# Kernel optimization log

Measured on AMD Instinct MI355X. Metric: run time of the kernel, lower is better.

Reference implementation:

```python
import jax, jax.numpy as jnp
import numpy as np

B, I, H = 16384, 512, 512
HH = H // 2


def _lrelu(v):
    return jnp.where(v > 0, v, 0.01 * v)


def setup_inputs() -> dict:
    key = jax.random.key(0)
    ks = jax.random.split(key, 20)
    s = 1.0 / np.sqrt(H)
    rn = lambda k, shp, sc: (jax.random.normal(k, shp, jnp.float32) * sc)
    return {
        "x": rn(ks[0], (B, I), 1.0),
        "h0": rn(ks[1], (1, B, H), 1.0),
        "c0": rn(ks[2], (1, B, H), 1.0),
        "cum": jax.random.uniform(ks[3], (B, 1), jnp.float32),
        # LSTM params (torch gate order i, f, g, o)
        "W_ih": rn(ks[4], (4 * H, I), s),
        "W_hh": rn(ks[5], (4 * H, H), s),
        "b_ih": rn(ks[6], (4 * H,), s),
        "b_hh": rn(ks[7], (4 * H,), s),
        # skip gate MLP
        "W_sp": rn(ks[8], (HH, H), s),
        "b_sp": rn(ks[9], (HH,), s),
        "W_sc": rn(ks[10], (HH, H), s),
        "b_sc": rn(ks[11], (HH,), s),
        "W_so": rn(ks[12], (1, HH), s),
        "b_so": rn(ks[13], (1,), s),
        # threshold gate MLP
        "W_tp": rn(ks[14], (HH, H), s),
        "b_tp": rn(ks[15], (HH,), s),
        "W_to": rn(ks[16], (1, HH), s),
        "b_to": rn(ks[17], (1,), s),
    }


def reference(x, h0, c0, cum, W_ih, W_hh, b_ih, b_hh,
              W_sp, b_sp, W_sc, b_sc, W_so, b_so,
              W_tp, b_tp, W_to, b_to):
    # single-step, single-layer LSTM
    gates = x @ W_ih.T + b_ih + h0[0] @ W_hh.T + b_hh  # [B, 4H]
    i_g, f_g, g_g, o_g = jnp.split(gates, 4, axis=-1)
    i_g = jax.nn.sigmoid(i_g)
    f_g = jax.nn.sigmoid(f_g)
    g_g = jnp.tanh(g_g)
    o_g = jax.nn.sigmoid(o_g)
    c1l = f_g * c0[0] + i_g * g_g          # [B, H]
    h1l = o_g * jnp.tanh(c1l)              # [B, H]
    h1, c1 = h1l[None], c1l[None]          # [1, B, H]

    # skip gate: delta prob from c0[-1], c1[-1]
    sg = _lrelu(c0[-1] @ W_sp.T + b_sp + c1[-1] @ W_sc.T + b_sc)  # [B, H/2]
    update_prob_delta = jax.nn.sigmoid(sg @ W_so.T + b_so)        # [B, 1]

    # threshold gate from c0[-1]
    tg = _lrelu(c0[-1] @ W_tp.T + b_tp)                           # [B, H/2]
    update_threshold = jax.nn.sigmoid(tg @ W_to.T + b_to)         # [B, 1]

    update_prob = cum + jnp.minimum(update_prob_delta, 1.0 - cum)  # [B, 1]
    # straight-through round: fwd hard threshold, bwd identity to prob
    hard = (update_prob > update_threshold).astype(jnp.float32)
    update_gate = update_prob + jax.lax.stop_gradient(hard - update_prob)

    new_h = update_gate * h1 + (1.0 - update_gate) * h0  # [1, B, H]
    new_c = update_gate * c1 + (1.0 - update_gate) * c0  # [1, B, H]
    update_cum = (1.0 - update_gate) * update_prob        # [B, 1]
    return (new_h, new_c, update_cum, update_prob_delta, update_prob)
```

## Files before the change

### kernel.cpp

```cpp
#include <hip/hip_runtime.h>
#include <math.h>

#define BB 16384
#define HH 512

typedef short short8 __attribute__((ext_vector_type(8)));
typedef float f32x4 __attribute__((ext_vector_type(4)));
typedef unsigned short ushort_t;

__device__ __forceinline__ float sigm(float v){ return 1.0f/(1.0f+expf(-v)); }

__device__ __forceinline__ unsigned short f2bf(float f){
    unsigned int u = __float_as_uint(f);
    u = u + 0x7FFFu + ((u>>16)&1u);
    return (unsigned short)(u>>16);
}
__device__ __forceinline__ float bf2f(unsigned short h){
    return __uint_as_float(((unsigned int)h)<<16);
}
__device__ __forceinline__ void gll16(const void* g, void* l){
    __builtin_amdgcn_global_load_lds((const __attribute__((address_space(1))) void*)g,
                                     (__attribute__((address_space(3))) void*)l, 16, 0, 0);
}

__global__ void k_prep_A(const float* __restrict__ x, const float* __restrict__ h0,
                         ushort_t* __restrict__ A1h, ushort_t* __restrict__ A1l)
{
    int u = blockIdx.x*256 + threadIdx.x;
    int r  = u & 255;
    int c  = (u >> 8) & 3;
    int kt = (u >> 10) & 31;
    int tm = u >> 15;
    int row = tm*256 + r;
    int k0 = kt*32 + c*8;
    const float* src = (k0 < 512) ? (x + (size_t)row*512 + k0)
                                  : (h0 + (size_t)row*512 + (k0-512));
    float4 v0 = *(const float4*)(src);
    float4 v1 = *(const float4*)(src+4);
    float vv[8] = {v0.x,v0.y,v0.z,v0.w,v1.x,v1.y,v1.z,v1.w};
    short8 hi, lo;
#pragma unroll
    for (int j=0;j<8;++j){
        unsigned short h = f2bf(vv[j]);
        unsigned short l = f2bf(vv[j] - bf2f(h));
        hi[j] = (short)h; lo[j] = (short)l;
    }
    size_t off = (size_t)u * 8;
    *(short8*)(A1h + off) = hi;
    *(short8*)(A1l + off) = lo;
}

__global__ void k_prep_A2(const float* __restrict__ c0,
                          ushort_t* __restrict__ A2h, ushort_t* __restrict__ A2l)
{
    int u = blockIdx.x*256 + threadIdx.x;
    int r  = u & 127;
    int c  = (u >> 7) & 3;
    int tk = (u >> 9) & 15;
    int tm = u >> 13;
    int row = tm*128 + r;
    int k0 = tk*32 + c*8;
    const float* src = c0 + (size_t)row*512 + k0;
    float4 v0 = *(const float4*)(src);
    float4 v1 = *(const float4*)(src+4);
    float vv[8] = {v0.x,v0.y,v0.z,v0.w,v1.x,v1.y,v1.z,v1.w};
    short8 hi, lo;
#pragma unroll
    for (int j=0;j<8;++j){
        unsigned short h = f2bf(vv[j]);
        unsigned short l = f2bf(vv[j] - bf2f(h));
        hi[j] = (short)h; lo[j] = (short)l;
    }
    size_t off = ((size_t)tm*32 + tk)*4096 + (size_t)(c*128 + r)*8;
    *(short8*)(A2h + off) = hi;
    *(short8*)(A2l + off) = lo;
}

__global__ void k_prep_B(const float* __restrict__ W_ih, const float* __restrict__ W_hh,
                         const float* __restrict__ b_ih, const float* __restrict__ b_hh,
                         ushort_t* __restrict__ B1h, ushort_t* __restrict__ B1l,
                         float* __restrict__ bgp)
{
    int u = blockIdx.x*256 + threadIdx.x;
    int r  = u & 255;
    int c  = (u >> 8) & 3;
    int kt = (u >> 10) & 31;
    int tn = u >> 15;
    int g = (r>>4)&3;
    int h = tn*64 + (r>>6)*16 + (r&15);
    int wrow = g*512 + h;
    int k0 = kt*32 + c*8;
    const float* src = (k0 < 512) ? (W_ih + (size_t)wrow*512 + k0)
                                  : (W_hh + (size_t)wrow*512 + (k0-512));
    float4 v0 = *(const float4*)(src);
    float4 v1 = *(const float4*)(src+4);
    float vv[8] = {v0.x,v0.y,v0.z,v0.w,v1.x,v1.y,v1.z,v1.w};
    short8 hi, lo;
#pragma unroll
    for (int j=0;j<8;++j){
        unsigned short hq = f2bf(vv[j]);
        unsigned short lq = f2bf(vv[j] - bf2f(hq));
        hi[j] = (short)hq; lo[j] = (short)lq;
    }
    size_t off = (size_t)u * 8;
    *(short8*)(B1h + off) = hi;
    *(short8*)(B1l + off) = lo;
    if (kt == 0 && c == 0) bgp[tn*256 + r] = b_ih[wrow] + b_hh[wrow];
}

__global__ void k_prep_B2(const float* __restrict__ W_sp, const float* __restrict__ W_sc,
                          const float* __restrict__ W_tp,
                          const float* __restrict__ b_sp, const float* __restrict__ b_sc,
                          const float* __restrict__ b_tp,
                          ushort_t* __restrict__ B2h, ushort_t* __restrict__ B2l,
                          float* __restrict__ bs2)
{
    int u = blockIdx.x*256 + threadIdx.x;
    int r  = u & 127;
    int c  = (u >> 7) & 3;
    int tk = (u >> 9) & 31;
    int tn = u >> 14;
    int n = tn*128 + r;
    int k0 = tk*32 + c*8;
    float vv[8];
    if (n < 256) {
        const float* src = (k0 < 512) ? (W_sp + (size_t)n*512 + k0)
                                      : (W_sc + (size_t)n*512 + (k0-512));
        float4 v0 = *(const float4*)(src);
        float4 v1 = *(const float4*)(src+4);
        vv[0]=v0.x; vv[1]=v0.y; vv[2]=v0.z; vv[3]=v0.w;
        vv[4]=v1.x; vv[5]=v1.y; vv[6]=v1.z; vv[7]=v1.w;
    } else if (k0 < 512) {
        const float* src = W_tp + (size_t)(n-256)*512 + k0;
        float4 v0 = *(const float4*)(src);
        float4 v1 = *(const float4*)(src+4);
        vv[0]=v0.x; vv[1]=v0.y; vv[2]=v0.z; vv[3]=v0.w;
        vv[4]=v1.x; vv[5]=v1.y; vv[6]=v1.z; vv[7]=v1.w;
    } else {
#pragma unroll
        for (int j=0;j<8;++j) vv[j] = 0.0f;
    }
    short8 hi, lo;
#pragma unroll
    for (int j=0;j<8;++j){
        unsigned short hq = f2bf(vv[j]);
        unsigned short lq = f2bf(vv[j] - bf2f(hq));
        hi[j] = (short)hq; lo[j] = (short)lq;
    }
    size_t off = (size_t)u * 8;
    *(short8*)(B2h + off) = hi;
    *(short8*)(B2l + off) = lo;
    if (tk == 0 && c == 0) bs2[n] = (n < 256) ? (b_sp[n] + b_sc[n]) : b_tp[n-256];
}

#define STEP(T, DO_STAGE, VMASM)                                                     \
  {                                                                                  \
    ushort_t* bufA = &lds[(T) & 3][0];                                               \
    ushort_t* bufB = &lds[(T) & 3][8192];                                            \
    short8 bf[4], af[4];                                                             \
    _Pragma("unroll") for (int fn = 0; fn < 4; ++fn)                                 \
        bf[fn] = *(const short8*)&bufB[boff[fn]];                                    \
    _Pragma("unroll") for (int fm = 0; fm < 4; ++fm)                                 \
        af[fm] = *(const short8*)&bufA[aoff[fm]];                                    \
    if (DO_STAGE) {                                                                  \
        const int uu = (T) + 3;                                                      \
        const ushort_t* As_ = ((uu >> 5) == 1) ? Al : Ah;                            \
        size_t ga = ((size_t)tm*32 + (uu & 31))*8192 + (size_t)tid*8;                \
        ushort_t* dA = &lds[uu & 3][0];                                              \
        gll16(As_ + ga,        dA + tid*8);                                          \
        gll16(As_ + ga + 4096, dA + 4096 + tid*8);                                   \
    }                                                                                \
    asm volatile("s_barrier" ::: "memory");                                          \
    asm volatile("s_waitcnt lgkmcnt(0)" ::: "memory");                               \
    __builtin_amdgcn_sched_barrier(0);                                               \
    __builtin_amdgcn_s_setprio(1);                                                   \
    _Pragma("unroll") for (int fm = 0; fm < 4; ++fm)                                 \
        _Pragma("unroll") for (int fn = 0; fn < 4; ++fn)                             \
            acc[fm][fn] = __builtin_amdgcn_mfma_f32_16x16x32_bf16(af[fm], bf[fn], acc[fm][fn], 0,0,0); \
    __builtin_amdgcn_s_setprio(0);                                                   \
    asm volatile("s_barrier" ::: "memory");                                          \
    short8 af2[4];                                                                   \
    _Pragma("unroll") for (int fm = 0; fm < 4; ++fm)                                 \
        af2[fm] = *(const short8*)&bufA[aoff[4+fm]];                                 \
    if (DO_STAGE) {                                                                  \
        const int uu = (T) + 3;                                                      \
        const ushort_t* Bs_ = ((uu >> 5) == 2) ? Bl : Bh;                            \
        size_t gb = ((size_t)tn*32 + (uu & 31))*8192 + (size_t)tid*8;                \
        ushort_t* dB = &lds[uu & 3][8192];                                           \
        gll16(Bs_ + gb,        dB + tid*8);                                          \
        gll16(Bs_ + gb + 4096, dB + 4096 + tid*8);                                   \
    }                                                                                \
    VMASM;                                                                           \
    asm volatile("s_barrier" ::: "memory");                                          \
    asm volatile("s_waitcnt lgkmcnt(0)" ::: "memory");                               \
    __builtin_amdgcn_sched_barrier(0);                                               \
    __builtin_amdgcn_s_setprio(1);                                                   \
    _Pragma("unroll") for (int fm = 0; fm < 4; ++fm)                                 \
        _Pragma("unroll") for (int fn = 0; fn < 4; ++fn)                             \
            acc[4+fm][fn] = __builtin_amdgcn_mfma_f32_16x16x32_bf16(af2[fm], bf[fn], acc[4+fm][fn], 0,0,0); \
    __builtin_amdgcn_s_setprio(0);                                                   \
    asm volatile("s_barrier" ::: "memory");                                          \
  }

__global__ __launch_bounds__(512, 2) void k_gemm_gates(
    const ushort_t* __restrict__ Ah, const ushort_t* __restrict__ Al,
    const ushort_t* __restrict__ Bh, const ushort_t* __restrict__ Bl,
    const float* __restrict__ bgp, const float* __restrict__ c0,
    float* __restrict__ outH, float* __restrict__ outC,
    ushort_t* __restrict__ A2h, ushort_t* __restrict__ A2l)
{
    __shared__ __align__(16) ushort_t lds[4][16384];
    const int tid  = threadIdx.x;
    const int lane = tid & 63;
    const int wid  = tid >> 6;
    const int wr   = wid >> 2;
    const int wc   = wid & 3;
    const int l15  = lane & 15;
    const int lq   = lane >> 4;
    const int bid  = (int)blockIdx.x;
    const int v    = (bid & 7)*64 + (bid >> 3);
    const int tm   = v >> 3;
    const int tn   = v & 7;

    f32x4 acc[8][4];
#pragma unroll
    for (int fn = 0; fn < 4; ++fn) {
        float bv = bgp[tn*256 + wc*64 + fn*16 + l15];
#pragma unroll
        for (int fm = 0; fm < 8; ++fm) {
            acc[fm][fn][0]=bv; acc[fm][fn][1]=bv; acc[fm][fn][2]=bv; acc[fm][fn][3]=bv;
        }
    }

    int aoff[8], boff[4];
#pragma unroll
    for (int f = 0; f < 8; ++f) aoff[f] = (lq*256 + wr*128 + f*16 + l15) * 8;
#pragma unroll
    for (int f = 0; f < 4; ++f) boff[f] = (lq*256 + wc*64 + f*16 + l15) * 8;

#pragma unroll
    for (int u0 = 0; u0 < 3; ++u0) {
        size_t ga = ((size_t)tm*32 + u0)*8192 + (size_t)tid*8;
        size_t gb = ((size_t)tn*32 + u0)*8192 + (size_t)tid*8;
        gll16(Ah + ga,        &lds[u0][0]     + tid*8);
        gll16(Ah + ga + 4096, &lds[u0][4096]  + tid*8);
        gll16(Bh + gb,        &lds[u0][8192]  + tid*8);
        gll16(Bh + gb + 4096, &lds[u0][12288] + tid*8);
    }
    asm volatile("s_waitcnt vmcnt(8)" ::: "memory");
    asm volatile("s_barrier" ::: "memory");

    for (int t = 0; t < 93; ++t) {
        STEP(t, 1, asm volatile("s_waitcnt vmcnt(8)" ::: "memory"));
    }
    STEP(93, 0, asm volatile("s_waitcnt vmcnt(4)" ::: "memory"));
    STEP(94, 0, asm volatile("s_waitcnt vmcnt(0)" ::: "memory"));
    STEP(95, 0, ((void)0));

    const int h = tn*64 + wc*16 + l15;
#pragma unroll
    for (int fm = 0; fm < 8; ++fm) {
        int row0 = tm*256 + wr*128 + fm*16 + lq*4;
#pragma unroll
        for (int r = 0; r < 4; ++r) {
            int row = row0 + r;
            size_t idx = (size_t)row*512 + h;
            float ig = sigm(acc[fm][0][r]);
            float fg = sigm(acc[fm][1][r]);
            float gg = tanhf(acc[fm][2][r]);
            float og = sigm(acc[fm][3][r]);
            float c1 = fg*c0[idx] + ig*gg;
            float h1 = og*tanhf(c1);
            outC[idx] = c1;
            outH[idx] = h1;
            unsigned short ch = f2bf(c1);
            unsigned short cl = f2bf(c1 - bf2f(ch));
            size_t a2 = ((size_t)(row>>7)*32 + 16 + (h>>5))*4096
                      + (size_t)((((h>>3)&3))*128 + (row&127))*8 + (h&7);
            A2h[a2] = ch;
            A2l[a2] = cl;
        }
    }
}

__global__ __launch_bounds__(256) void k_gemm_sgtg(
    const ushort_t* __restrict__ Ah, const ushort_t* __restrict__ Al,
    const ushort_t* __restrict__ Bh, const ushort_t* __restrict__ Bl,
    const float* __restrict__ bs2,
    float* __restrict__ sgtg)
{
    __shared__ __align__(16) ushort_t AsH[4096];
    __shared__ __align__(16) ushort_t AsL[4096];
    __shared__ __align__(16) ushort_t BsH[4096];
    __shared__ __align__(16) ushort_t BsL[4096];
    const int tid = threadIdx.x;
    const int lane = tid & 63;
    const int wid = tid >> 6;
    const int wr = wid >> 1, wc = wid & 1;
    const int bid = (int)blockIdx.x;
    const int v = (bid & 7)*64 + (bid >> 3);
    const int tm = v >> 2;
    const int tn = v & 3;
    const int l15 = lane & 15;
    const int lq = lane >> 4;

    f32x4 acc[4][4];
#pragma unroll
    for (int fn = 0; fn < 4; ++fn) {
        float bv = bs2[tn*128 + wc*64 + fn*16 + l15];
#pragma unroll
        for (int fm = 0; fm < 4; ++fm) {
            acc[fm][fn][0]=bv; acc[fm][fn][1]=bv; acc[fm][fn][2]=bv; acc[fm][fn][3]=bv;
        }
    }

    const size_t baseA = (size_t)tm * (32*4096);
    const size_t baseB = (size_t)tn * (32*4096);
    int aoff[4], boff[4];
#pragma unroll
    for (int f = 0; f < 4; ++f) {
        aoff[f] = (lq*128 + wr*64 + f*16 + l15) * 8;
        boff[f] = (lq*128 + wc*64 + f*16 + l15) * 8;
    }
    const int si = wid * 2;

    for (int tk = 0; tk < 32; ++tk) {
        size_t ga = baseA + (size_t)tk*4096 + (size_t)lane*8;
        size_t gb = baseB + (size_t)tk*4096 + (size_t)lane*8;
#pragma unroll
        for (int t = 0; t < 2; ++t) {
            int i = si + t;
            gll16(Ah + ga + i*512, AsH + i*512);
            gll16(Al + ga + i*512, AsL + i*512);
            gll16(Bh + gb + i*512, BsH + i*512);
            gll16(Bl + gb + i*512, BsL + i*512);
        }
        __syncthreads();
        short8 bhv[4], blv[4];
#pragma unroll
        for (int fn = 0; fn < 4; ++fn) {
            bhv[fn] = *(const short8*)&BsH[boff[fn]];
            blv[fn] = *(const short8*)&BsL[boff[fn]];
        }
#pragma unroll
        for (int fm = 0; fm < 4; ++fm) {
            short8 ahv = *(const short8*)&AsH[aoff[fm]];
            short8 alv = *(const short8*)&AsL[aoff[fm]];
#pragma unroll
            for (int fn = 0; fn < 4; ++fn) {
                acc[fm][fn] = __builtin_amdgcn_mfma_f32_16x16x32_bf16(ahv, bhv[fn], acc[fm][fn], 0,0,0);
                acc[fm][fn] = __builtin_amdgcn_mfma_f32_16x16x32_bf16(alv, bhv[fn], acc[fm][fn], 0,0,0);
                acc[fm][fn] = __builtin_amdgcn_mfma_f32_16x16x32_bf16(ahv, blv[fn], acc[fm][fn], 0,0,0);
            }
        }
        __syncthreads();
    }

#pragma unroll
    for (int fm = 0; fm < 4; ++fm) {
        int row0 = tm*128 + wr*64 + fm*16 + lq*4;
#pragma unroll
        for (int fn = 0; fn < 4; ++fn) {
            int n = tn*128 + wc*64 + fn*16 + l15;
#pragma unroll
            for (int r = 0; r < 4; ++r) {
                int row = row0 + r;
                float vv = acc[fm][fn][r];
                vv = vv > 0.f ? vv : 0.01f*vv;
                sgtg[(size_t)row*512 + n] = vv;
            }
        }
    }
}

__global__ __launch_bounds__(256) void k_final(
    const float* __restrict__ sgtg,
    const float* __restrict__ h0, const float* __restrict__ c0,
    const float* __restrict__ cum,
    const float* __restrict__ W_so, const float* __restrict__ b_so,
    const float* __restrict__ W_to, const float* __restrict__ b_to,
    float* __restrict__ outH, float* __restrict__ outC,
    float* __restrict__ outCum, float* __restrict__ outDelta, float* __restrict__ outProb)
{
    int w = threadIdx.x >> 6;
    int lane = threadIdx.x & 63;
    int b = blockIdx.x * 4 + w;
    const float* row = sgtg + (size_t)b * 512;
    float so = 0.f, to = 0.f;
#pragma unroll
    for (int u = 0; u < 4; ++u) {
        int c = lane + 64 * u;
        so = fmaf(row[c], W_so[c], so);
        to = fmaf(row[256 + c], W_to[c], to);
    }
#pragma unroll
    for (int off = 32; off; off >>= 1) {
        so += __shfl_down(so, off);
        to += __shfl_down(to, off);
    }
    so = __shfl(so, 0);
    to = __shfl(to, 0);
    float delta = sigm(so + b_so[0]);
    float thr   = sigm(to + b_to[0]);
    float cu = cum[b];
    float prob = cu + fminf(delta, 1.0f - cu);
    float hard = (prob > thr) ? 1.0f : 0.0f;
    if (lane == 0) {
        outDelta[b] = delta;
        outProb[b]  = prob;
        outCum[b]   = (1.0f - hard) * prob;
    }
    if (hard == 0.0f) {
#pragma unroll
        for (int u = 0; u < 8; ++u) {
            size_t idx = (size_t)b * 512 + lane + 64 * u;
            outH[idx] = h0[idx];
            outC[idx] = c0[idx];
        }
    }
}

extern "C" void kernel_launch(void* const* d_in, const int* in_sizes, int n_in,
                              void* d_out, int out_size, void* d_ws, size_t ws_size,
                              hipStream_t stream)
{
    const float* x    = (const float*)d_in[0];
    const float* h0   = (const float*)d_in[1];
    const float* c0   = (const float*)d_in[2];
    const float* cum  = (const float*)d_in[3];
    const float* W_ih = (const float*)d_in[4];
    const float* W_hh = (const float*)d_in[5];
    const float* b_ih = (const float*)d_in[6];
    const float* b_hh = (const float*)d_in[7];
    const float* W_sp = (const float*)d_in[8];
    const float* b_sp = (const float*)d_in[9];
    const float* W_sc = (const float*)d_in[10];
    const float* b_sc = (const float*)d_in[11];
    const float* W_so = (const float*)d_in[12];
    const float* b_so = (const float*)d_in[13];
    const float* W_tp = (const float*)d_in[14];
    const float* b_tp = (const float*)d_in[15];
    const float* W_to = (const float*)d_in[16];
    const float* b_to = (const float*)d_in[17];

    float* out      = (float*)d_out;
    float* outH     = out;
    float* outC     = out + (size_t)BB * HH;
    float* outCum   = out + (size_t)2 * BB * HH;
    float* outDelta = outCum + BB;
    float* outProb  = outDelta + BB;

    char* w = (char*)d_ws;
    ushort_t* A1h = (ushort_t*)(w);
    ushort_t* A1l = (ushort_t*)(w + 33554432ull);
    ushort_t* A2h = (ushort_t*)(w + 67108864ull);
    ushort_t* A2l = (ushort_t*)(w + 100663296ull);
    ushort_t* B1h = (ushort_t*)(w + 134217728ull);
    ushort_t* B1l = (ushort_t*)(w + 138412032ull);
    ushort_t* B2h = (ushort_t*)(w + 142606336ull);
    ushort_t* B2l = (ushort_t*)(w + 143654912ull);
    float*    bgp = (float*)(w + 144703488ull);
    float*    bs2 = (float*)(w + 144711680ull);
    float*    sgtg = (float*)A1h;

    k_prep_A <<<8192, 256, 0, stream>>>(x, h0, A1h, A1l);
    k_prep_A2<<<4096, 256, 0, stream>>>(c0, A2h, A2l);
    k_prep_B <<<1024, 256, 0, stream>>>(W_ih, W_hh, b_ih, b_hh, B1h, B1l, bgp);
    k_prep_B2<<<256, 256, 0, stream>>>(W_sp, W_sc, W_tp, b_sp, b_sc, b_tp, B2h, B2l, bs2);
    k_gemm_gates<<<512, 512, 0, stream>>>(A1h, A1l, B1h, B1l, bgp, c0,
                                          outH, outC, A2h, A2l);
    k_gemm_sgtg<<<512, 256, 0, stream>>>(A2h, A2l, B2h, B2l, bs2, sgtg);
    k_final<<<4096, 256, 0, stream>>>(sgtg, h0, c0, cum, W_so, b_so, W_to, b_to,
                                      outH, outC, outCum, outDelta, outProb);
}
```

Baseline: 349.2 us.

## Merge prep kernels, single-phase gates step, and pipeline sgtg GEMM with 4-stage LDS ring

Fuses the four bf16 hi/lo split prep kernels into one launch dispatched by block range, cutting launch overhead. The gates GEMM step now loads all 8 A fragments at once and issues A and B staging together, leaving one barrier-separated MFMA phase per step instead of two. The sgtg GEMM is rebuilt in the same style as the gates GEMM: a K-split stream of 96 steps (hi, lo-A, lo-B) with a 4-deep global_load_lds ring and launch_bounds(256,2), replacing the synchronous per-tile loop that used 3 MFMAs per step. The trade-off is more registers for the fragments in the gates kernel and more LDS in sgtg (64 KB), which may limit occupancy.

```diff
diff --git a/kernel.cpp b/kernel.cpp
--- a/kernel.cpp
+++ b/kernel.cpp
@@ -22,171 +22,127 @@
     __builtin_amdgcn_global_load_lds((const __attribute__((address_space(1))) void*)g,
                                      (__attribute__((address_space(3))) void*)l, 16, 0, 0);
 }
-
-__global__ void k_prep_A(const float* __restrict__ x, const float* __restrict__ h0,
-                         ushort_t* __restrict__ A1h, ushort_t* __restrict__ A1l)
+__device__ __forceinline__ void split_store(float v, ushort_t* ph, ushort_t* pl, int j){
+    unsigned short h = f2bf(v);
+    unsigned short l = f2bf(v - bf2f(h));
+    ph[j] = h; pl[j] = l;
+}
+
+__global__ void k_prep_all(
+    const float* __restrict__ x, const float* __restrict__ h0, const float* __restrict__ c0,
+    const float* __restrict__ W_ih, const float* __restrict__ W_hh,
+    const float* __restrict__ b_ih, const float* __restrict__ b_hh,
+    const float* __restrict__ W_sp, const float* __restrict__ W_sc, const float* __restrict__ W_tp,
+    const float* __restrict__ b_sp, const float* __restrict__ b_sc, const float* __restrict__ b_tp,
+    ushort_t* __restrict__ A1h, ushort_t* __restrict__ A1l,
+    ushort_t* __restrict__ A2h, ushort_t* __restrict__ A2l,
+    ushort_t* __restrict__ B1h, ushort_t* __restrict__ B1l,
+    ushort_t* __restrict__ B2h, ushort_t* __restrict__ B2l,
+    float* __restrict__ bgp, float* __restrict__ bs2)
 {
-    int u = blockIdx.x*256 + threadIdx.x;
-    int r  = u & 255;
-    int c  = (u >> 8) & 3;
-    int kt = (u >> 10) & 31;
-    int tm = u >> 15;
-    int row = tm*256 + r;
-    int k0 = kt*32 + c*8;
-    const float* src = (k0 < 512) ? (x + (size_t)row*512 + k0)
-                                  : (h0 + (size_t)row*512 + (k0-512));
-    float4 v0 = *(const float4*)(src);
-    float4 v1 = *(const float4*)(src+4);
-    float vv[8] = {v0.x,v0.y,v0.z,v0.w,v1.x,v1.y,v1.z,v1.w};
-    short8 hi, lo;
-#pragma unroll
-    for (int j=0;j<8;++j){
-        unsigned short h = f2bf(vv[j]);
-        unsigned short l = f2bf(vv[j] - bf2f(h));
-        hi[j] = (short)h; lo[j] = (short)l;
-    }
-    size_t off = (size_t)u * 8;
-    *(short8*)(A1h + off) = hi;
-    *(short8*)(A1l + off) = lo;
-}
-
-__global__ void k_prep_A2(const float* __restrict__ c0,
-                          ushort_t* __restrict__ A2h, ushort_t* __restrict__ A2l)
-{
-    int u = blockIdx.x*256 + threadIdx.x;
-    int r  = u & 127;
-    int c  = (u >> 7) & 3;
-    int tk = (u >> 9) & 15;
-    int tm = u >> 13;
-    int row = tm*128 + r;
-    int k0 = tk*32 + c*8;
-    const float* src = c0 + (size_t)row*512 + k0;
-    float4 v0 = *(const float4*)(src);
-    float4 v1 = *(const float4*)(src+4);
-    float vv[8] = {v0.x,v0.y,v0.z,v0.w,v1.x,v1.y,v1.z,v1.w};
-    short8 hi, lo;
-#pragma unroll
-    for (int j=0;j<8;++j){
-        unsigned short h = f2bf(vv[j]);
-        unsigned short l = f2bf(vv[j] - bf2f(h));
-        hi[j] = (short)h; lo[j] = (short)l;
-    }
-    size_t off = ((size_t)tm*32 + tk)*4096 + (size_t)(c*128 + r)*8;
-    *(short8*)(A2h + off) = hi;
-    *(short8*)(A2l + off) = lo;
-}
-
-__global__ void k_prep_B(const float* __restrict__ W_ih, const float* __restrict__ W_hh,
-                         const float* __restrict__ b_ih, const float* __restrict__ b_hh,
-                         ushort_t* __restrict__ B1h, ushort_t* __restrict__ B1l,
-                         float* __restrict__ bgp)
-{
-    int u = blockIdx.x*256 + threadIdx.x;
-    int r  = u & 255;
-    int c  = (u >> 8) & 3;
-    int kt = (u >> 10) & 31;
-    int tn = u >> 15;
-    int g = (r>>4)&3;
-    int h = tn*64 + (r>>6)*16 + (r&15);
-    int wrow = g*512 + h;
-    int k0 = kt*32 + c*8;
-    const float* src = (k0 < 512) ? (W_ih + (size_t)wrow*512 + k0)
-                                  : (W_hh + (size_t)wrow*512 + (k0-512));
-    float4 v0 = *(const float4*)(src);
-    float4 v1 = *(const float4*)(src+4);
-    float vv[8] = {v0.x,v0.y,v0.z,v0.w,v1.x,v1.y,v1.z,v1.w};
-    short8 hi, lo;
-#pragma unroll
-    for (int j=0;j<8;++j){
-        unsigned short hq = f2bf(vv[j]);
-        unsigned short lq = f2bf(vv[j] - bf2f(hq));
-        hi[j] = (short)hq; lo[j] = (short)lq;
-    }
-    size_t off = (size_t)u * 8;
-    *(short8*)(B1h + off) = hi;
-    *(short8*)(B1l + off) = lo;
-    if (kt == 0 && c == 0) bgp[tn*256 + r] = b_ih[wrow] + b_hh[wrow];
-}
-
-__global__ void k_prep_B2(const float* __restrict__ W_sp, const float* __restrict__ W_sc,
-                          const float* __restrict__ W_tp,
-                          const float* __restrict__ b_sp, const float* __restrict__ b_sc,
-                          const float* __restrict__ b_tp,
-                          ushort_t* __restrict__ B2h, ushort_t* __restrict__ B2l,
-                          float* __restrict__ bs2)
-{
-    int u = blockIdx.x*256 + threadIdx.x;
-    int r  = u & 127;
-    int c  = (u >> 7) & 3;
-    int tk = (u >> 9) & 31;
-    int tn = u >> 14;
-    int n = tn*128 + r;
-    int k0 = tk*32 + c*8;
-    float vv[8];
-    if (n < 256) {
-        const float* src = (k0 < 512) ? (W_sp + (size_t)n*512 + k0)
-                                      : (W_sc + (size_t)n*512 + (k0-512));
+    int bid = blockIdx.x;
+    if (bid < 8192) {
+        int u = bid*256 + threadIdx.x;
+        int r  = u & 255;
+        int c  = (u >> 8) & 3;
+        int kt = (u >> 10) & 31;
+        int tm = u >> 15;
+        int row = tm*256 + r;
+        int k0 = kt*32 + c*8;
+        const float* src = (k0 < 512) ? (x + (size_t)row*512 + k0)
+                                      : (h0 + (size_t)row*512 + (k0-512));
         float4 v0 = *(const float4*)(src);
         float4 v1 = *(const float4*)(src+4);
-        vv[0]=v0.x; vv[1]=v0.y; vv[2]=v0.z; vv[3]=v0.w;
-        vv[4]=v1.x; vv[5]=v1.y; vv[6]=v1.z; vv[7]=v1.w;
-    } else if (k0 < 512) {
-        const float* src = W_tp + (size_t)(n-256)*512 + k0;
+        float vv[8] = {v0.x,v0.y,v0.z,v0.w,v1.x,v1.y,v1.z,v1.w};
+        size_t off = (size_t)u * 8;
+#pragma unroll
+        for (int j=0;j<8;++j) split_store(vv[j], A1h+off, A1l+off, j);
+    } else if (bid < 12288) {
+        int u = (bid-8192)*256 + threadIdx.x;
+        int r  = u & 127;
+        int c  = (u >> 7) & 3;
+        int tk = (u >> 9) & 15;
+        int tm = u >> 13;
+        int row = tm*128 + r;
+        int k0 = tk*32 + c*8;
+        const float* src = c0 + (size_t)row*512 + k0;
         float4 v0 = *(const float4*)(src);
         float4 v1 = *(const float4*)(src+4);
-        vv[0]=v0.x; vv[1]=v0.y; vv[2]=v0.z; vv[3]=v0.w;
-        vv[4]=v1.x; vv[5]=v1.y; vv[6]=v1.z; vv[7]=v1.w;
+        float vv[8] = {v0.x,v0.y,v0.z,v0.w,v1.x,v1.y,v1.z,v1.w};
+        size_t off = ((size_t)tm*32 + tk)*4096 + (size_t)(c*128 + r)*8;
+#pragma unroll
+        for (int j=0;j<8;++j) split_store(vv[j], A2h+off, A2l+off, j);
+    } else if (bid < 13312) {
+        int u = (bid-12288)*256 + threadIdx.x;
+        int r  = u & 255;
+        int c  = (u >> 8) & 3;
+        int kt = (u >> 10) & 31;
+        int tn = u >> 15;
+        int g = (r>>4)&3;
+        int h = tn*64 + (r>>6)*16 + (r&15);
+        int wrow = g*512 + h;
+        int k0 = kt*32 + c*8;
+        const float* src = (k0 < 512) ? (W_ih + (size_t)wrow*512 + k0)
+                                      : (W_hh + (size_t)wrow*512 + (k0-512));
+        float4 v0 = *(const float4*)(src);
+        float4 v1 = *(const float4*)(src+4);
+        float vv[8] = {v0.x,v0.y,v0.z,v0.w,v1.x,v1.y,v1.z,v1.w};
+        size_t off = (size_t)u * 8;
+#pragma unroll
+        for (int j=0;j<8;++j) split_store(vv[j], B1h+off, B1l+off, j);
+        if (kt == 0 && c == 0) bgp[tn*256 + r] = b_ih[wrow] + b_hh[wrow];
     } else {
-#pragma unroll
-        for (int j=0;j<8;++j) vv[j] = 0.0f;
-    }
-    short8 hi, lo;
-#pragma unroll
-    for (int j=0;j<8;++j){
-        unsigned short hq = f2bf(vv[j]);
-        unsigned short lq = f2bf(vv[j] - bf2f(hq));
-        hi[j] = (short)hq; lo[j] = (short)lq;
-    }
-    size_t off = (size_t)u * 8;
-    *(short8*)(B2h + off) = hi;
-    *(short8*)(B2l + off) = lo;
-    if (tk == 0 && c == 0) bs2[n] = (n < 256) ? (b_sp[n] + b_sc[n]) : b_tp[n-256];
-}
-
-#define STEP(T, DO_STAGE, VMASM)                                                     \
+        int u = (bid-13312)*256 + threadIdx.x;
+        int r  = u & 127;
+        int c  = (u >> 7) & 3;
+        int tk = (u >> 9) & 31;
+        int tn = u >> 14;
+        int n = tn*128 + r;
+        int k0 = tk*32 + c*8;
+        float vv[8];
+        if (n < 256) {
+            const float* src = (k0 < 512) ? (W_sp + (size_t)n*512 + k0)
+                                          : (W_sc + (size_t)n*512 + (k0-512));
+            float4 v0 = *(const float4*)(src);
+            float4 v1 = *(const float4*)(src+4);
+            vv[0]=v0.x; vv[1]=v0.y; vv[2]=v0.z; vv[3]=v0.w;
+            vv[4]=v1.x; vv[5]=v1.y; vv[6]=v1.z; vv[7]=v1.w;
+        } else if (k0 < 512) {
+            const float* src = W_tp + (size_t)(n-256)*512 + k0;
+            float4 v0 = *(const float4*)(src);
+            float4 v1 = *(const float4*)(src+4);
+            vv[0]=v0.x; vv[1]=v0.y; vv[2]=v0.z; vv[3]=v0.w;
+            vv[4]=v1.x; vv[5]=v1.y; vv[6]=v1.z; vv[7]=v1.w;
+        } else {
+#pragma unroll
+            for (int j=0;j<8;++j) vv[j] = 0.0f;
+        }
+        size_t off = (size_t)u * 8;
+#pragma unroll
+        for (int j=0;j<8;++j) split_store(vv[j], B2h+off, B2l+off, j);
+        if (tk == 0 && c == 0) bs2[n] = (n < 256) ? (b_sp[n] + b_sc[n]) : b_tp[n-256];
+    }
+}
+
+#define STEPG(T, DO_STAGE, VMASM)                                                    \
   {                                                                                  \
     ushort_t* bufA = &lds[(T) & 3][0];                                               \
     ushort_t* bufB = &lds[(T) & 3][8192];                                            \
-    short8 bf[4], af[4];                                                             \
-    _Pragma("unroll") for (int fn = 0; fn < 4; ++fn)                                 \
-        bf[fn] = *(const short8*)&bufB[boff[fn]];                                    \
-    _Pragma("unroll") for (int fm = 0; fm < 4; ++fm)                                 \
-        af[fm] = *(const short8*)&bufA[aoff[fm]];                                    \
+    short8 af[8], bf[4];                                                             \
+    _Pragma("unroll") for (int f = 0; f < 8; ++f)                                    \
+        af[f] = *(const short8*)&bufA[aoff[f]];                                      \
+    _Pragma("unroll") for (int f = 0; f < 4; ++f)                                    \
+        bf[f] = *(const short8*)&bufB[boff[f]];                                      \
     if (DO_STAGE) {                                                                  \
         const int uu = (T) + 3;                                                      \
         const ushort_t* As_ = ((uu >> 5) == 1) ? Al : Ah;                            \
+        const ushort_t* Bs_ = ((uu >> 5) == 2) ? Bl : Bh;                            \
         size_t ga = ((size_t)tm*32 + (uu & 31))*8192 + (size_t)tid*8;                \
+        size_t gb = ((size_t)tn*32 + (uu & 31))*8192 + (size_t)tid*8;                \
         ushort_t* dA = &lds[uu & 3][0];                                              \
+        ushort_t* dB = &lds[uu & 3][8192];                                           \
         gll16(As_ + ga,        dA + tid*8);                                          \
         gll16(As_ + ga + 4096, dA + 4096 + tid*8);                                   \
-    }                                                                                \
-    asm volatile("s_barrier" ::: "memory");                                          \
-    asm volatile("s_waitcnt lgkmcnt(0)" ::: "memory");                               \
-    __builtin_amdgcn_sched_barrier(0);                                               \
-    __builtin_amdgcn_s_setprio(1);                                                   \
-    _Pragma("unroll") for (int fm = 0; fm < 4; ++fm)                                 \
-        _Pragma("unroll") for (int fn = 0; fn < 4; ++fn)                             \
-            acc[fm][fn] = __builtin_amdgcn_mfma_f32_16x16x32_bf16(af[fm], bf[fn], acc[fm][fn], 0,0,0); \
-    __builtin_amdgcn_s_setprio(0);                                                   \
-    asm volatile("s_barrier" ::: "memory");                                          \
-    short8 af2[4];                                                                   \
-    _Pragma("unroll") for (int fm = 0; fm < 4; ++fm)                                 \
-        af2[fm] = *(const short8*)&bufA[aoff[4+fm]];                                 \
-    if (DO_STAGE) {                                                                  \
-        const int uu = (T) + 3;                                                      \
-        const ushort_t* Bs_ = ((uu >> 5) == 2) ? Bl : Bh;                            \
-        size_t gb = ((size_t)tn*32 + (uu & 31))*8192 + (size_t)tid*8;                \
-        ushort_t* dB = &lds[uu & 3][8192];                                           \
         gll16(Bs_ + gb,        dB + tid*8);                                          \
         gll16(Bs_ + gb + 4096, dB + 4096 + tid*8);                                   \
     }                                                                                \
@@ -195,9 +151,9 @@
     asm volatile("s_waitcnt lgkmcnt(0)" ::: "memory");                               \
     __builtin_amdgcn_sched_barrier(0);                                               \
     __builtin_amdgcn_s_setprio(1);                                                   \
-    _Pragma("unroll") for (int fm = 0; fm < 4; ++fm)                                 \
+    _Pragma("unroll") for (int fm = 0; fm < 8; ++fm)                                 \
         _Pragma("unroll") for (int fn = 0; fn < 4; ++fn)                             \
-            acc[4+fm][fn] = __builtin_amdgcn_mfma_f32_16x16x32_bf16(af2[fm], bf[fn], acc[4+fm][fn], 0,0,0); \
+            acc[fm][fn] = __builtin_amdgcn_mfma_f32_16x16x32_bf16(af[fm], bf[fn], acc[fm][fn], 0,0,0); \
     __builtin_amdgcn_s_setprio(0);                                                   \
     asm volatile("s_barrier" ::: "memory");                                          \
   }
@@ -251,11 +207,11 @@
     asm volatile("s_barrier" ::: "memory");
 
     for (int t = 0; t < 93; ++t) {
-        STEP(t, 1, asm volatile("s_waitcnt vmcnt(8)" ::: "memory"));
-    }
-    STEP(93, 0, asm volatile("s_waitcnt vmcnt(4)" ::: "memory"));
-    STEP(94, 0, asm volatile("s_waitcnt vmcnt(0)" ::: "memory"));
-    STEP(95, 0, ((void)0));
+        STEPG(t, 1, asm volatile("s_waitcnt vmcnt(8)" ::: "memory"));
+    }
+    STEPG(93, 0, asm volatile("s_waitcnt vmcnt(4)" ::: "memory"));
+    STEPG(94, 0, asm volatile("s_waitcnt vmcnt(0)" ::: "memory"));
+    STEPG(95, 0, ((void)0));
 
     const int h = tn*64 + wc*16 + l15;
 #pragma unroll
@@ -283,26 +239,58 @@
     }
 }
 
-__global__ __launch_bounds__(256) void k_gemm_sgtg(
+#define STEPS(T, DO_STAGE, VMASM)                                                    \
+  {                                                                                  \
+    ushort_t* bufA = &lds2[(T) & 3][0];                                              \
+    ushort_t* bufB = &lds2[(T) & 3][4096];                                           \
+    short8 af[4], bf[4];                                                             \
+    _Pragma("unroll") for (int f = 0; f < 4; ++f)                                    \
+        af[f] = *(const short8*)&bufA[aoff[f]];                                      \
+    _Pragma("unroll") for (int f = 0; f < 4; ++f)                                    \
+        bf[f] = *(const short8*)&bufB[boff[f]];                                      \
+    if (DO_STAGE) {                                                                  \
+        const int uu = (T) + 3;                                                      \
+        const ushort_t* As_ = ((uu >> 5) == 1) ? Al : Ah;                            \
+        const ushort_t* Bs_ = ((uu >> 5) == 2) ? Bl : Bh;                            \
+        size_t ga = ((size_t)tm*32 + (uu & 31))*4096 + (size_t)tid*8;                \
+        size_t gb = ((size_t)tn*32 + (uu & 31))*4096 + (size_t)tid*8;                \
+        ushort_t* dA = &lds2[uu & 3][0];                                             \
+        ushort_t* dB = &lds2[uu & 3][4096];                                          \
+        gll16(As_ + ga,        dA + tid*8);                                          \
+        gll16(As_ + ga + 2048, dA + 2048 + tid*8);                                   \
+        gll16(Bs_ + gb,        dB + tid*8);                                          \
+        gll16(Bs_ + gb + 2048, dB + 2048 + tid*8);                                   \
+    }                                                                                \
+    VMASM;                                                                           \
+    asm volatile("s_barrier" ::: "memory");                                          \
+    asm volatile("s_waitcnt lgkmcnt(0)" ::: "memory");                               \
+    __builtin_amdgcn_sched_barrier(0);                                               \
+    __builtin_amdgcn_s_setprio(1);                                                   \
+    _Pragma("unroll") for (int fm = 0; fm < 4; ++fm)                                 \
+        _Pragma("unroll") for (int fn = 0; fn < 4; ++fn)                             \
+            acc[fm][fn] = __builtin_amdgcn_mfma_f32_16x16x32_bf16(af[fm], bf[fn], acc[fm][fn], 0,0,0); \
+    __builtin_amdgcn_s_setprio(0);                                                   \
+    asm volatile("s_barrier" ::: "memory");                                          \
+  }
+
+__global__ __launch_bounds__(256, 2) void k_gemm_sgtg(
     const ushort_t* __restrict__ Ah, const ushort_t* __restrict__ Al,
     const ushort_t* __restrict__ Bh, const ushort_t* __restrict__ Bl,
     const float* __restrict__ bs2,
     float* __restrict__ sgtg)
 {
-    __shared__ __align__(16) ushort_t AsH[4096];
-    __shared__ __align__(16) ushort_t AsL[4096];
-    __shared__ __align__(16) ushort_t BsH[4096];
-    __shared__ __align__(16) ushort_t BsL[4096];
-    const int tid = threadIdx.x;
+    __shared__ __align__(16) ushort_t lds2[4][8192];
+    const int tid  = threadIdx.x;
     const int lane = tid & 63;
-    const int wid = tid >> 6;
-    const int wr = wid >> 1, wc = wid & 1;
-    const int bid = (int)blockIdx.x;
-    const int v = (bid & 7)*64 + (bid >> 3);
-    const int tm = v >> 2;
-    const int tn = v & 3;
-    const int l15 = lane & 15;
-    const int lq = lane >> 4;
+    const int wid  = tid >> 6;
+    const int wr   = wid >> 1;
+    const int wc   = wid & 1;
+    const int l15  = lane & 15;
+    const int lq   = lane >> 4;
+    const int bid  = (int)blockIdx.x;
+    const int v    = (bid & 7)*64 + (bid >> 3);
+    const int tm   = v >> 2;
+    const int tn   = v & 3;
 
     f32x4 acc[4][4];
 #pragma unroll
@@ -314,47 +302,31 @@
         }
     }
 
-    const size_t baseA = (size_t)tm * (32*4096);
-    const size_t baseB = (size_t)tn * (32*4096);
     int aoff[4], boff[4];
 #pragma unroll
     for (int f = 0; f < 4; ++f) {
         aoff[f] = (lq*128 + wr*64 + f*16 + l15) * 8;
         boff[f] = (lq*128 + wc*64 + f*16 + l15) * 8;
     }
-    const int si = wid * 2;
-
-    for (int tk = 0; tk < 32; ++tk) {
-        size_t ga = baseA + (size_t)tk*4096 + (size_t)lane*8;
-        size_t gb = baseB + (size_t)tk*4096 + (size_t)lane*8;
-#pragma unroll
-        for (int t = 0; t < 2; ++t) {
-            int i = si + t;
-            gll16(Ah + ga + i*512, AsH + i*512);
-            gll16(Al + ga + i*512, AsL + i*512);
-            gll16(Bh + gb + i*512, BsH + i*512);
-            gll16(Bl + gb + i*512, BsL + i*512);
-        }
-        __syncthreads();
-        short8 bhv[4], blv[4];
-#pragma unroll
-        for (int fn = 0; fn < 4; ++fn) {
-            bhv[fn] = *(const short8*)&BsH[boff[fn]];
-            blv[fn] = *(const short8*)&BsL[boff[fn]];
-        }
-#pragma unroll
-        for (int fm = 0; fm < 4; ++fm) {
-            short8 ahv = *(const short8*)&AsH[aoff[fm]];
-            short8 alv = *(const short8*)&AsL[aoff[fm]];
-#pragma unroll
-            for (int fn = 0; fn < 4; ++fn) {
-                acc[fm][fn] = __builtin_amdgcn_mfma_f32_16x16x32_bf16(ahv, bhv[fn], acc[fm][fn], 0,0,0);
-                acc[fm][fn] = __builtin_amdgcn_mfma_f32_16x16x32_bf16(alv, bhv[fn], acc[fm][fn], 0,0,0);
-                acc[fm][fn] = __builtin_amdgcn_mfma_f32_16x16x32_bf16(ahv, blv[fn], acc[fm][fn], 0,0,0);
-            }
-        }
-        __syncthreads();
-    }
+
+#pragma unroll
+    for (int u0 = 0; u0 < 3; ++u0) {
+        size_t ga = ((size_t)tm*32 + u0)*4096 + (size_t)tid*8;
+        size_t gb = ((size_t)tn*32 + u0)*4096 + (size_t)tid*8;
+        gll16(Ah + ga,        &lds2[u0][0]    + tid*8);
+        gll16(Ah + ga + 2048, &lds2[u0][2048] + tid*8);
+        gll16(Bh + gb,        &lds2[u0][4096] + tid*8);
+        gll16(Bh + gb + 2048, &lds2[u0][6144] + tid*8);
+    }
+    asm volatile("s_waitcnt vmcnt(8)" ::: "memory");
+    asm volatile("s_barrier" ::: "memory");
+
+    for (int t = 0; t < 93; ++t) {
+        STEPS(t, 1, asm volatile("s_waitcnt vmcnt(8)" ::: "memory"));
+    }
+    STEPS(93, 0, asm volatile("s_waitcnt vmcnt(4)" ::: "memory"));
+    STEPS(94, 0, asm volatile("s_waitcnt vmcnt(0)" ::: "memory"));
+    STEPS(95, 0, ((void)0));
 
 #pragma unroll
     for (int fm = 0; fm < 4; ++fm) {
@@ -463,10 +435,10 @@
     float*    bs2 = (float*)(w + 144711680ull);
     float*    sgtg = (float*)A1h;
 
-    k_prep_A <<<8192, 256, 0, stream>>>(x, h0, A1h, A1l);
-    k_prep_A2<<<4096, 256, 0, stream>>>(c0, A2h, A2l);
-    k_prep_B <<<1024, 256, 0, stream>>>(W_ih, W_hh, b_ih, b_hh, B1h, B1l, bgp);
-    k_prep_B2<<<256, 256, 0, stream>>>(W_sp, W_sc, W_tp, b_sp, b_sc, b_tp, B2h, B2l, bs2);
+    k_prep_all<<<13568, 256, 0, stream>>>(x, h0, c0, W_ih, W_hh, b_ih, b_hh,
+                                          W_sp, W_sc, W_tp, b_sp, b_sc, b_tp,
+                                          A1h, A1l, A2h, A2l, B1h, B1l, B2h, B2l,
+                                          bgp, bs2);
     k_gemm_gates<<<512, 512, 0, stream>>>(A1h, A1l, B1h, B1l, bgp, c0,
                                           outH, outC, A2h, A2l);
     k_gemm_sgtg<<<512, 256, 0, stream>>>(A2h, A2l, B2h, B2l, bs2, sgtg);
```

Result: no change. 350.9 us (+0.5%).
